# Kernel optimization log

Hardware: AMD Instinct MI355X
Metric: run time of the kernel (lower is better)

The kernel has to match this reference:

```python
import jax, jax.numpy as jnp
import numpy as np

B, S, DIM, H, DH = 2, 2048, 1024, 16, 64
INNER = H * DH


def setup_inputs() -> dict:
    key = jax.random.key(0)
    ks = jax.random.split(key, 4)
    sd = 0.02
    return {
        "x": jax.random.normal(ks[0], (B, S, DIM), dtype=jnp.float32),
        "ln_w": jnp.ones((DIM,), jnp.float32),
        "ln_b": jnp.zeros((DIM,), jnp.float32),
        "Wq": jax.random.normal(ks[1], (DIM, INNER), jnp.float32) * sd,
        "Wkv": jax.random.normal(ks[2], (DIM, 2 * INNER), jnp.float32) * sd,
        "q_gamma": jnp.ones((H, 1, DH), jnp.float32),
        "k_gamma": jnp.ones((H, 1, DH), jnp.float32),
        "Wo": jax.random.normal(ks[3], (INNER, DIM), jnp.float32) * sd,
    }


def _rmsnorm(t, gamma, scale):
    # t: (b,h,s,d); gamma: (h,1,d)
    normed = t * jax.lax.rsqrt(jnp.mean(t * t, axis=-1, keepdims=True) + 1e-8)
    return normed * scale * gamma


def reference(x, ln_w, ln_b, Wq, Wkv, q_gamma, k_gamma, Wo):
    h, dh = q_gamma.shape[0], q_gamma.shape[-1]
    b, s, _ = x.shape
    # pre-LayerNorm (eps 1e-5, biased variance)
    mean = jnp.mean(x, axis=-1, keepdims=True)
    var = jnp.var(x, axis=-1, keepdims=True)
    xn = ln_w * (x - mean) / jnp.sqrt(var + 1e-5) + ln_b
    # projections
    q = xn @ Wq                       # (b,s,h*dh)
    k, v = jnp.split(xn @ Wkv, 2, axis=-1)
    # split heads -> (b,h,s,dh)
    to_heads = lambda t: t.reshape(b, s, h, dh).transpose(0, 2, 1, 3)
    q, k, v = to_heads(q), to_heads(k), to_heads(v)
    scale = dh ** 0.5
    q = _rmsnorm(q, q_gamma, scale)
    k = _rmsnorm(k, k_gamma, scale)
    # attention (no extra 1/sqrt(d): RMSNorm scale already applied)
    dots = jnp.einsum("bhid,bhjd->bhij", q, k)
    attn = jax.nn.softmax(dots, axis=-1)
    out = jnp.einsum("bhij,bhjd->bhid", attn, v)
    out = out.transpose(0, 2, 1, 3).reshape(b, s, h * dh)
    return out @ Wo
```

## Files before the change

kernel.cpp:

```cpp
#include <hip/hip_runtime.h>
#include <hip/hip_bf16.h>

#define DEVFN __device__ __forceinline__

typedef __attribute__((ext_vector_type(8))) short short8;
typedef __attribute__((ext_vector_type(4))) short short4v;
typedef __attribute__((ext_vector_type(4))) float f32x4;

#define MFMA(a,b,c) __builtin_amdgcn_mfma_f32_16x16x32_bf16((a),(b),(c),0,0,0)

DEVFN void gload_lds16(const __hip_bfloat16* g, __hip_bfloat16* l) {
  __builtin_amdgcn_global_load_lds((const __attribute__((address_space(1))) void*)g,
                                   (__attribute__((address_space(3))) void*)l, 16, 0, 0);
}

DEVFN float bf2f(__hip_bfloat16 h) { return __bfloat162float(h); }
DEVFN __hip_bfloat16 f2bf(float f) { return __float2bfloat16(f); }

DEVFN void store_out(float* p, float v) { *p = v; }
DEVFN void store_out(__hip_bfloat16* p, float v) { *p = f2bf(v); }

__global__ __launch_bounds__(256) void ln_split_kernel(
    const float* __restrict__ x, const float* __restrict__ lw, const float* __restrict__ lb,
    __hip_bfloat16* __restrict__ xh, __hip_bfloat16* __restrict__ xl) {
  int row = blockIdx.x, t = threadIdx.x;
  float4 v = ((const float4*)(x + (size_t)row * 1024))[t];
  float s  = v.x + v.y + v.z + v.w;
  float ss = v.x*v.x + v.y*v.y + v.z*v.z + v.w*v.w;
  #pragma unroll
  for (int m = 1; m < 64; m <<= 1) { s += __shfl_xor(s, m); ss += __shfl_xor(ss, m); }
  __shared__ float red[8];
  int wv = t >> 6;
  if ((t & 63) == 0) { red[wv] = s; red[4 + wv] = ss; }
  __syncthreads();
  s  = red[0] + red[1] + red[2] + red[3];
  ss = red[4] + red[5] + red[6] + red[7];
  float mean = s * (1.f/1024.f);
  float var  = ss * (1.f/1024.f) - mean*mean;
  float inv  = rsqrtf(var + 1e-5f);
  float4 wv4 = ((const float4*)lw)[t];
  float4 bv4 = ((const float4*)lb)[t];
  float xv[4] = {v.x, v.y, v.z, v.w};
  float wa[4] = {wv4.x, wv4.y, wv4.z, wv4.w};
  float ba[4] = {bv4.x, bv4.y, bv4.z, bv4.w};
  union { short4v s4; __hip_bfloat16 h[4]; } uh, ul;
  #pragma unroll
  for (int j = 0; j < 4; ++j) {
    float val = (xv[j] - mean) * inv * wa[j] + ba[j];
    __hip_bfloat16 hi = f2bf(val);
    uh.h[j] = hi;
    ul.h[j] = f2bf(val - bf2f(hi));
  }
  ((short4v*)(xh + (size_t)row * 1024))[t] = uh.s4;
  ((short4v*)(xl + (size_t)row * 1024))[t] = ul.s4;
}

__global__ __launch_bounds__(256) void wprep_kernel(
    const float* __restrict__ Wq, const float* __restrict__ Wkv, const float* __restrict__ Wo,
    __hip_bfloat16* __restrict__ Wqk_h, __hip_bfloat16* __restrict__ Wqk_l,
    __hip_bfloat16* __restrict__ Wv, __hip_bfloat16* __restrict__ Wot) {
  __shared__ float tile[64][68];
  int bid = blockIdx.x, t = threadIdx.x;
  const float* src; int srcN, kt, nt, drow;
  __hip_bfloat16 *dh, *dl;
  if (bid < 256) {
    src = Wq; srcN = 1024; kt = bid >> 4; nt = bid & 15;
    dh = Wqk_h; dl = Wqk_l; drow = nt * 64;
  } else if (bid < 768) {
    int r = bid - 256; src = Wkv; srcN = 2048; kt = r >> 5; nt = r & 31;
    if (nt < 16) { dh = Wqk_h; dl = Wqk_l; drow = 1024 + nt * 64; }
    else         { dh = Wv;    dl = nullptr; drow = (nt - 16) * 64; }
  } else {
    int r = bid - 768; src = Wo; srcN = 1024; kt = r >> 4; nt = r & 15;
    dh = Wot; dl = nullptr; drow = nt * 64;
  }
  int lr = t >> 2, c = t & 3;
  const float* sp = src + (size_t)(kt*64 + lr) * srcN + nt*64 + c*16;
  float* tr = &tile[lr][c*16];
  ((float4*)tr)[0] = ((const float4*)sp)[0];
  ((float4*)tr)[1] = ((const float4*)sp)[1];
  ((float4*)tr)[2] = ((const float4*)sp)[2];
  ((float4*)tr)[3] = ((const float4*)sp)[3];
  __syncthreads();
  union { short8 s8[2]; __hip_bfloat16 h[16]; } hh, ll;
  #pragma unroll
  for (int e = 0; e < 16; ++e) {
    float wv = tile[c*16 + e][lr];
    __hip_bfloat16 hi = f2bf(wv);
    hh.h[e] = hi;
    ll.h[e] = f2bf(wv - bf2f(hi));
  }
  size_t doff = (size_t)(drow + lr) * 1024 + kt*64 + c*16;
  ((short8*)(dh + doff))[0] = hh.s8[0];
  ((short8*)(dh + doff))[1] = hh.s8[1];
  if (dl) {
    ((short8*)(dl + doff))[0] = ll.s8[0];
    ((short8*)(dl + doff))[1] = ll.s8[1];
  }
}

__global__ __launch_bounds__(256) void gemm_dual_kernel(
    const __hip_bfloat16* __restrict__ Ah, const __hip_bfloat16* __restrict__ Al,
    const __hip_bfloat16* __restrict__ Bh, const __hip_bfloat16* __restrict__ Bl,
    __hip_bfloat16* __restrict__ Ch, __hip_bfloat16* __restrict__ Cl,
    const float* __restrict__ qg, const float* __restrict__ kg) {
  __shared__ __align__(16) __hip_bfloat16 sAh[128*32], sAl[128*32], sBh[128*32], sBl[128*32];
  const int K = 1024, N = 2048;
  int mt = blockIdx.x, nt = blockIdx.y;
  int t = threadIdx.x, w = t >> 6, l = t & 63;
  int wr = w >> 1, wc = w & 1, lr = l & 15, lk = (l >> 4) * 8;
  f32x4 acc[4][4] = {};
  for (int k0 = 0; k0 < K; k0 += 32) {
    #pragma unroll
    for (int i = 0; i < 2; ++i) {
      int ci = i*256 + t;
      size_t ga = (size_t)(mt*128 + (ci >> 2)) * K + k0 + (ci & 3) * 8;
      size_t gb = (size_t)(nt*128 + (ci >> 2)) * K + k0 + (ci & 3) * 8;
      int ldst = (i*256 + w*64) * 8;
      gload_lds16(Ah + ga, sAh + ldst);
      gload_lds16(Al + ga, sAl + ldst);
      gload_lds16(Bh + gb, sBh + ldst);
      gload_lds16(Bl + gb, sBl + ldst);
    }
    __syncthreads();
    short8 ah[4], al[4], bh[4], bl[4];
    #pragma unroll
    for (int m = 0; m < 4; ++m) {
      int ro = (wr*64 + m*16 + lr)*32 + lk;
      ah[m] = *(const short8*)(sAh + ro);
      al[m] = *(const short8*)(sAl + ro);
    }
    #pragma unroll
    for (int n = 0; n < 4; ++n) {
      int ro = (wc*64 + n*16 + lr)*32 + lk;
      bh[n] = *(const short8*)(sBh + ro);
      bl[n] = *(const short8*)(sBl + ro);
    }
    #pragma unroll
    for (int m = 0; m < 4; ++m)
      #pragma unroll
      for (int n = 0; n < 4; ++n) {
        acc[m][n] = MFMA(ah[m], bh[n], acc[m][n]);
        acc[m][n] = MFMA(ah[m], bl[n], acc[m][n]);
        acc[m][n] = MFMA(al[m], bh[n], acc[m][n]);
      }
    __syncthreads();
  }
  int col0 = nt*128 + wc*64;
  int head = col0 >> 6;
  const float* gamma = (head < 16) ? (qg + head*64) : (kg + (head - 16)*64);
  float g[4];
  #pragma unroll
  for (int nf = 0; nf < 4; ++nf) g[nf] = gamma[nf*16 + lr];
  #pragma unroll
  for (int m = 0; m < 4; ++m) {
    #pragma unroll
    for (int r = 0; r < 4; ++r) {
      float ss2 = 0.f;
      #pragma unroll
      for (int nf = 0; nf < 4; ++nf) ss2 += acc[m][nf][r] * acc[m][nf][r];
      #pragma unroll
      for (int msk = 1; msk < 16; msk <<= 1) ss2 += __shfl_xor(ss2, msk);
      float scl = rsqrtf(ss2 * (1.f/64.f) + 1e-8f) * 8.f;
      int row = mt*128 + wr*64 + m*16 + (l >> 4)*4 + r;
      #pragma unroll
      for (int nf = 0; nf < 4; ++nf) {
        float val = acc[m][nf][r] * scl * g[nf];
        __hip_bfloat16 hi = f2bf(val);
        size_t off = (size_t)row * N + col0 + nf*16 + lr;
        Ch[off] = hi;
        Cl[off] = f2bf(val - bf2f(hi));
      }
    }
  }
}

template <typename OUT_T>
__global__ __launch_bounds__(256) void gemm_single_kernel(
    const __hip_bfloat16* __restrict__ A, const __hip_bfloat16* __restrict__ Bt,
    OUT_T* __restrict__ C, int N) {
  __shared__ __align__(16) __hip_bfloat16 sA[128*32], sB[128*32];
  const int K = 1024;
  int mt = blockIdx.x, nt = blockIdx.y;
  int t = threadIdx.x, w = t >> 6, l = t & 63;
  int wr = w >> 1, wc = w & 1, lr = l & 15, lk = (l >> 4) * 8;
  f32x4 acc[4][4] = {};
  for (int k0 = 0; k0 < K; k0 += 32) {
    #pragma unroll
    for (int i = 0; i < 2; ++i) {
      int ci = i*256 + t;
      size_t ga = (size_t)(mt*128 + (ci >> 2)) * K + k0 + (ci & 3) * 8;
      size_t gb = (size_t)(nt*128 + (ci >> 2)) * K + k0 + (ci & 3) * 8;
      int ldst = (i*256 + w*64) * 8;
      gload_lds16(A + ga, sA + ldst);
      gload_lds16(Bt + gb, sB + ldst);
    }
    __syncthreads();
    short8 af[4], bf[4];
    #pragma unroll
    for (int m = 0; m < 4; ++m) af[m] = *(const short8*)(sA + (wr*64 + m*16 + lr)*32 + lk);
    #pragma unroll
    for (int n = 0; n < 4; ++n) bf[n] = *(const short8*)(sB + (wc*64 + n*16 + lr)*32 + lk);
    #pragma unroll
    for (int m = 0; m < 4; ++m)
      #pragma unroll
      for (int n = 0; n < 4; ++n)
        acc[m][n] = MFMA(af[m], bf[n], acc[m][n]);
    __syncthreads();
  }
  int row0 = mt*128 + wr*64, col0 = nt*128 + wc*64;
  #pragma unroll
  for (int m = 0; m < 4; ++m)
    #pragma unroll
    for (int n = 0; n < 4; ++n)
      #pragma unroll
      for (int r = 0; r < 4; ++r) {
        int row = row0 + m*16 + (l >> 4)*4 + r;
        int col = col0 + n*16 + lr;
        store_out(&C[(size_t)row * N + col], acc[m][n][r]);
      }
}

__global__ __launch_bounds__(256) void attn_kernel(
    const __hip_bfloat16* __restrict__ qk_h, const __hip_bfloat16* __restrict__ qk_l,
    const __hip_bfloat16* __restrict__ vbuf, __hip_bfloat16* __restrict__ ao) {
  __shared__ __align__(16) __hip_bfloat16 sKh[64*72], sKl[64*72], sVt[64*72];
  __shared__ __align__(16) __hip_bfloat16 sP[4][16*72];
  int t = threadIdx.x, w = t >> 6, l = t & 63, lr = l & 15, lk = (l >> 4) * 8;
  int bh = blockIdx.x >> 5, qt = blockIdx.x & 31;
  int b = bh >> 4, h = bh & 15;
  const __hip_bfloat16* qbh = qk_h + (size_t)b * 2048 * 2048 + h * 64;
  const __hip_bfloat16* qbl = qk_l + (size_t)b * 2048 * 2048 + h * 64;
  const __hip_bfloat16* kbh = qbh + 1024;
  const __hip_bfloat16* kbl = qbl + 1024;
  const __hip_bfloat16* vb  = vbuf + (size_t)b * 2048 * 1024 + h * 64;
  int qrow = qt*64 + w*16 + lr;
  short8 qh0 = *(const short8*)(qbh + (size_t)qrow*2048 + lk);
  short8 qh1 = *(const short8*)(qbh + (size_t)qrow*2048 + 32 + lk);
  short8 ql0 = *(const short8*)(qbl + (size_t)qrow*2048 + lk);
  short8 ql1 = *(const short8*)(qbl + (size_t)qrow*2048 + 32 + lk);
  f32x4 o_acc[4] = {};
  float m_run[4], l_run[4];
  #pragma unroll
  for (int r = 0; r < 4; ++r) { m_run[r] = -1e30f; l_run[r] = 0.f; }

  for (int kv0 = 0; kv0 < 2048; kv0 += 64) {
    {
      int j = t >> 2, c = t & 3;
      size_t go = (size_t)(kv0 + j) * 2048 + c * 16;
      const short8* gkh = (const short8*)(kbh + go);
      const short8* gkl = (const short8*)(kbl + go);
      *(short8*)(sKh + j*72 + c*16)     = gkh[0];
      *(short8*)(sKh + j*72 + c*16 + 8) = gkh[1];
      *(short8*)(sKl + j*72 + c*16)     = gkl[0];
      *(short8*)(sKl + j*72 + c*16 + 8) = gkl[1];
      const short8* gv = (const short8*)(vb + (size_t)(kv0 + j) * 1024 + c * 16);
      union { short8 s8[2]; __hip_bfloat16 hh[16]; } uv;
      uv.s8[0] = gv[0];
      uv.s8[1] = gv[1];
      #pragma unroll
      for (int e = 0; e < 16; ++e) sVt[(c*16 + e)*72 + j] = uv.hh[e];
    }
    __syncthreads();
    f32x4 s_acc[4];
    #pragma unroll
    for (int nf = 0; nf < 4; ++nf) {
      int ro = (nf*16 + lr) * 72;
      short8 kh0 = *(const short8*)(sKh + ro + lk);
      short8 kh1 = *(const short8*)(sKh + ro + 32 + lk);
      short8 kl0 = *(const short8*)(sKl + ro + lk);
      short8 kl1 = *(const short8*)(sKl + ro + 32 + lk);
      f32x4 sa = {};
      sa = MFMA(qh0, kh0, sa);
      sa = MFMA(qh1, kh1, sa);
      sa = MFMA(qh0, kl0, sa);
      sa = MFMA(qh1, kl1, sa);
      sa = MFMA(ql0, kh0, sa);
      sa = MFMA(ql1, kh1, sa);
      s_acc[nf] = sa;
    }
    #pragma unroll
    for (int r = 0; r < 4; ++r) {
      float mx = fmaxf(fmaxf(s_acc[0][r], s_acc[1][r]), fmaxf(s_acc[2][r], s_acc[3][r]));
      #pragma unroll
      for (int msk = 1; msk < 16; msk <<= 1) mx = fmaxf(mx, __shfl_xor(mx, msk));
      float mnew = fmaxf(m_run[r], mx);
      float corr = __expf(m_run[r] - mnew);
      m_run[r] = mnew;
      float rowsum = 0.f;
      #pragma unroll
      for (int nf = 0; nf < 4; ++nf) {
        float pv = __expf(s_acc[nf][r] - mnew);
        __hip_bfloat16 pb = f2bf(pv);
        sP[w][((l >> 4)*4 + r)*72 + nf*16 + lr] = pb;
        rowsum += bf2f(pb);
      }
      #pragma unroll
      for (int msk = 1; msk < 16; msk <<= 1) rowsum += __shfl_xor(rowsum, msk);
      l_run[r] = l_run[r] * corr + rowsum;
      #pragma unroll
      for (int df = 0; df < 4; ++df) o_acc[df][r] *= corr;
    }
    #pragma unroll
    for (int kk = 0; kk < 2; ++kk) {
      short8 pf = *(const short8*)(&sP[w][lr*72 + kk*32 + lk]);
      #pragma unroll
      for (int df = 0; df < 4; ++df) {
        short8 vf = *(const short8*)(sVt + (df*16 + lr)*72 + kk*32 + lk);
        o_acc[df] = MFMA(pf, vf, o_acc[df]);
      }
    }
    __syncthreads();
  }
  size_t orow0 = (size_t)b*2048 + qt*64 + w*16 + (l >> 4)*4;
  #pragma unroll
  for (int df = 0; df < 4; ++df)
    #pragma unroll
    for (int r = 0; r < 4; ++r) {
      float oval = o_acc[df][r] / l_run[r];
      ao[(orow0 + r) * 1024 + h*64 + df*16 + lr] = f2bf(oval);
    }
}

extern "C" void kernel_launch(void* const* d_in, const int* in_sizes, int n_in,
                              void* d_out, int out_size, void* d_ws, size_t ws_size,
                              hipStream_t stream) {
  const float* x   = (const float*)d_in[0];
  const float* lw  = (const float*)d_in[1];
  const float* lb  = (const float*)d_in[2];
  const float* Wq  = (const float*)d_in[3];
  const float* Wkv = (const float*)d_in[4];
  const float* qg  = (const float*)d_in[5];
  const float* kg  = (const float*)d_in[6];
  const float* Wo  = (const float*)d_in[7];
  float* out = (float*)d_out;
  char* ws = (char*)d_ws;
  const size_t MB = 1024 * 1024;
  __hip_bfloat16* xh    = (__hip_bfloat16*)(ws + 0);
  __hip_bfloat16* xl    = (__hip_bfloat16*)(ws + 8*MB);
  __hip_bfloat16* qk_h  = (__hip_bfloat16*)(ws + 16*MB);
  __hip_bfloat16* qk_l  = (__hip_bfloat16*)(ws + 32*MB);
  __hip_bfloat16* Wqk_h = (__hip_bfloat16*)(ws + 48*MB);
  __hip_bfloat16* Wqk_l = (__hip_bfloat16*)(ws + 52*MB);
  __hip_bfloat16* Wv    = (__hip_bfloat16*)(ws + 56*MB);
  __hip_bfloat16* Wot   = (__hip_bfloat16*)(ws + 58*MB);
  __hip_bfloat16* vbuf  = (__hip_bfloat16*)(ws + 8*MB);
  __hip_bfloat16* ao    = (__hip_bfloat16*)(ws + 0);

  ln_split_kernel<<<4096, 256, 0, stream>>>(x, lw, lb, xh, xl);
  wprep_kernel<<<1024, 256, 0, stream>>>(Wq, Wkv, Wo, Wqk_h, Wqk_l, Wv, Wot);
  gemm_dual_kernel<<<dim3(32, 16), 256, 0, stream>>>(xh, xl, Wqk_h, Wqk_l, qk_h, qk_l, qg, kg);
  gemm_single_kernel<__hip_bfloat16><<<dim3(32, 8), 256, 0, stream>>>(xh, Wv, vbuf, 1024);
  attn_kernel<<<1024, 256, 0, stream>>>(qk_h, qk_l, vbuf, ao);
  gemm_single_kernel<float><<<dim3(32, 8), 256, 0, stream>>>(ao, Wot, out, 1024);
}
```

Before: 357.1 us.

## Pre-transpose V and use direct global-to-LDS loads with XOR swizzle in attention

Adds a separate kernel that transposes V per head into a contiguous [d][s] layout. The attention kernel can then stage K_hi, K_lo and V^T tiles with global_load_lds DMA instead of register round-trips and scalar transposed LDS stores. The padded LDS layout is replaced by an XOR-swizzled layout for K, V and P to avoid bank conflicts, and block ordering changes so that query tiles of the same head are spread across blocks. The cost is an extra kernel launch and an extra pass over V in memory.

```diff
diff --git a/kernel.cpp b/kernel.cpp
--- a/kernel.cpp
+++ b/kernel.cpp
@@ -221,19 +221,38 @@
       }
 }
 
+__global__ __launch_bounds__(256) void vtrans_kernel(
+    const __hip_bfloat16* __restrict__ vbuf, __hip_bfloat16* __restrict__ vT) {
+  __shared__ __hip_bfloat16 tile[64][72];
+  int bid = blockIdx.x;
+  int b = bid >> 9, h = (bid >> 5) & 15, st = bid & 31;
+  int t = threadIdx.x, j = t >> 2, c = t & 3;
+  const short8* src = (const short8*)(vbuf + (size_t)(b*2048 + st*64 + j) * 1024 + h*64 + c*16);
+  *(short8*)&tile[j][c*16]     = src[0];
+  *(short8*)&tile[j][c*16 + 8] = src[1];
+  __syncthreads();
+  int d = t >> 2, c2 = t & 3;
+  union { short8 s8[2]; __hip_bfloat16 hh[16]; } o;
+  #pragma unroll
+  for (int e = 0; e < 16; ++e) o.hh[e] = tile[c2*16 + e][d];
+  short8* dst = (short8*)(vT + (size_t)((b*16 + h)*64 + d) * 2048 + st*64 + c2*16);
+  dst[0] = o.s8[0];
+  dst[1] = o.s8[1];
+}
+
 __global__ __launch_bounds__(256) void attn_kernel(
     const __hip_bfloat16* __restrict__ qk_h, const __hip_bfloat16* __restrict__ qk_l,
-    const __hip_bfloat16* __restrict__ vbuf, __hip_bfloat16* __restrict__ ao) {
-  __shared__ __align__(16) __hip_bfloat16 sKh[64*72], sKl[64*72], sVt[64*72];
-  __shared__ __align__(16) __hip_bfloat16 sP[4][16*72];
-  int t = threadIdx.x, w = t >> 6, l = t & 63, lr = l & 15, lk = (l >> 4) * 8;
-  int bh = blockIdx.x >> 5, qt = blockIdx.x & 31;
+    const __hip_bfloat16* __restrict__ vT, __hip_bfloat16* __restrict__ ao) {
+  __shared__ __align__(16) __hip_bfloat16 sKh[64*64], sKl[64*64], sVt[64*64];
+  __shared__ __align__(16) __hip_bfloat16 sP[4*16*64];
+  int t = threadIdx.x, w = t >> 6, l = t & 63, lr = l & 15, hi = l >> 4, lk = hi * 8;
+  int bh = blockIdx.x & 31, qt = blockIdx.x >> 5;
   int b = bh >> 4, h = bh & 15;
   const __hip_bfloat16* qbh = qk_h + (size_t)b * 2048 * 2048 + h * 64;
   const __hip_bfloat16* qbl = qk_l + (size_t)b * 2048 * 2048 + h * 64;
   const __hip_bfloat16* kbh = qbh + 1024;
   const __hip_bfloat16* kbl = qbl + 1024;
-  const __hip_bfloat16* vb  = vbuf + (size_t)b * 2048 * 1024 + h * 64;
+  const __hip_bfloat16* vtb = vT + (size_t)bh * 64 * 2048;
   int qrow = qt*64 + w*16 + lr;
   short8 qh0 = *(const short8*)(qbh + (size_t)qrow*2048 + lk);
   short8 qh1 = *(const short8*)(qbh + (size_t)qrow*2048 + 32 + lk);
@@ -244,32 +263,30 @@
   #pragma unroll
   for (int r = 0; r < 4; ++r) { m_run[r] = -1e30f; l_run[r] = 0.f; }
 
+  int swl = lr & 7;
+  int c0e = (hi ^ swl) << 3;
+  int c1e = c0e ^ 32;
+  int ci0 = t, ci1 = 256 + t;
+  int r0 = ci0 >> 3, cs0 = (ci0 & 7) ^ (r0 & 7);
+  int r1 = ci1 >> 3, cs1 = (ci1 & 7) ^ (r1 & 7);
+  int ldb0 = (w*64) * 8, ldb1 = (256 + w*64) * 8;
+
   for (int kv0 = 0; kv0 < 2048; kv0 += 64) {
-    {
-      int j = t >> 2, c = t & 3;
-      size_t go = (size_t)(kv0 + j) * 2048 + c * 16;
-      const short8* gkh = (const short8*)(kbh + go);
-      const short8* gkl = (const short8*)(kbl + go);
-      *(short8*)(sKh + j*72 + c*16)     = gkh[0];
-      *(short8*)(sKh + j*72 + c*16 + 8) = gkh[1];
-      *(short8*)(sKl + j*72 + c*16)     = gkl[0];
-      *(short8*)(sKl + j*72 + c*16 + 8) = gkl[1];
-      const short8* gv = (const short8*)(vb + (size_t)(kv0 + j) * 1024 + c * 16);
-      union { short8 s8[2]; __hip_bfloat16 hh[16]; } uv;
-      uv.s8[0] = gv[0];
-      uv.s8[1] = gv[1];
-      #pragma unroll
-      for (int e = 0; e < 16; ++e) sVt[(c*16 + e)*72 + j] = uv.hh[e];
-    }
+    gload_lds16(kbh + (size_t)(kv0 + r0)*2048 + cs0*8, sKh + ldb0);
+    gload_lds16(kbh + (size_t)(kv0 + r1)*2048 + cs1*8, sKh + ldb1);
+    gload_lds16(kbl + (size_t)(kv0 + r0)*2048 + cs0*8, sKl + ldb0);
+    gload_lds16(kbl + (size_t)(kv0 + r1)*2048 + cs1*8, sKl + ldb1);
+    gload_lds16(vtb + (size_t)r0*2048 + kv0 + cs0*8, sVt + ldb0);
+    gload_lds16(vtb + (size_t)r1*2048 + kv0 + cs1*8, sVt + ldb1);
     __syncthreads();
     f32x4 s_acc[4];
     #pragma unroll
     for (int nf = 0; nf < 4; ++nf) {
-      int ro = (nf*16 + lr) * 72;
-      short8 kh0 = *(const short8*)(sKh + ro + lk);
-      short8 kh1 = *(const short8*)(sKh + ro + 32 + lk);
-      short8 kl0 = *(const short8*)(sKl + ro + lk);
-      short8 kl1 = *(const short8*)(sKl + ro + 32 + lk);
+      int rb = (nf*16 + lr) * 64;
+      short8 kh0 = *(const short8*)(sKh + rb + c0e);
+      short8 kh1 = *(const short8*)(sKh + rb + c1e);
+      short8 kl0 = *(const short8*)(sKl + rb + c0e);
+      short8 kl1 = *(const short8*)(sKl + rb + c1e);
       f32x4 sa = {};
       sa = MFMA(qh0, kh0, sa);
       sa = MFMA(qh1, kh1, sa);
@@ -287,12 +304,15 @@
       float mnew = fmaxf(m_run[r], mx);
       float corr = __expf(m_run[r] - mnew);
       m_run[r] = mnew;
+      int prow = hi*4 + r;
+      int pbase = (w << 10) + prow*64 + (swl );
       float rowsum = 0.f;
       #pragma unroll
       for (int nf = 0; nf < 4; ++nf) {
         float pv = __expf(s_acc[nf][r] - mnew);
         __hip_bfloat16 pb = f2bf(pv);
-        sP[w][((l >> 4)*4 + r)*72 + nf*16 + lr] = pb;
+        int chunk = (nf << 1) | (lr >> 3);
+        sP[pbase + ((chunk ^ (prow & 7)) << 3)] = pb;
         rowsum += bf2f(pb);
       }
       #pragma unroll
@@ -303,16 +323,17 @@
     }
     #pragma unroll
     for (int kk = 0; kk < 2; ++kk) {
-      short8 pf = *(const short8*)(&sP[w][lr*72 + kk*32 + lk]);
+      int vck = (((kk << 2) | hi) ^ swl) << 3;
+      short8 pf = *(const short8*)(sP + (w << 10) + lr*64 + vck);
       #pragma unroll
       for (int df = 0; df < 4; ++df) {
-        short8 vf = *(const short8*)(sVt + (df*16 + lr)*72 + kk*32 + lk);
+        short8 vf = *(const short8*)(sVt + (df*16 + lr)*64 + vck);
         o_acc[df] = MFMA(pf, vf, o_acc[df]);
       }
     }
     __syncthreads();
   }
-  size_t orow0 = (size_t)b*2048 + qt*64 + w*16 + (l >> 4)*4;
+  size_t orow0 = (size_t)b*2048 + qt*64 + w*16 + hi*4;
   #pragma unroll
   for (int df = 0; df < 4; ++df)
     #pragma unroll
@@ -344,6 +365,7 @@
   __hip_bfloat16* Wqk_l = (__hip_bfloat16*)(ws + 52*MB);
   __hip_bfloat16* Wv    = (__hip_bfloat16*)(ws + 56*MB);
   __hip_bfloat16* Wot   = (__hip_bfloat16*)(ws + 58*MB);
+  __hip_bfloat16* vT    = (__hip_bfloat16*)(ws + 60*MB);
   __hip_bfloat16* vbuf  = (__hip_bfloat16*)(ws + 8*MB);
   __hip_bfloat16* ao    = (__hip_bfloat16*)(ws + 0);
 
@@ -351,6 +373,7 @@
   wprep_kernel<<<1024, 256, 0, stream>>>(Wq, Wkv, Wo, Wqk_h, Wqk_l, Wv, Wot);
   gemm_dual_kernel<<<dim3(32, 16), 256, 0, stream>>>(xh, xl, Wqk_h, Wqk_l, qk_h, qk_l, qg, kg);
   gemm_single_kernel<__hip_bfloat16><<<dim3(32, 8), 256, 0, stream>>>(xh, Wv, vbuf, 1024);
-  attn_kernel<<<1024, 256, 0, stream>>>(qk_h, qk_l, vbuf, ao);
+  vtrans_kernel<<<1024, 256, 0, stream>>>(vbuf, vT);
+  attn_kernel<<<1024, 256, 0, stream>>>(qk_h, qk_l, vT, ao);
   gemm_single_kernel<float><<<dim3(32, 8), 256, 0, stream>>>(ao, Wot, out, 1024);
 }
```

Measured after the change: 335.2 us. 6.1% less time.
